# Performance work log

Hardware: AMD Instinct MI355X
Metric: run time of the kernel (lower is better)

## Reference

```python
import jax, jax.numpy as jnp
import numpy as np

H, KD, VD, KNN = 8, 64, 64, 128
D, FC, N, S = 512, 2048, 4, 1024
GW_DEC, GW_ENC = 0.5, 0.5
EPS = 1e-5
SCALE = float(np.sqrt(KD))


def _layer_norm(x):
    # nn.LayerNorm(out_dim, eps=1e-5, elementwise_affine=False)
    m = jnp.mean(x, -1, keepdims=True)
    v = jnp.var(x, -1, keepdims=True)
    return (x - m) * jax.lax.rsqrt(v + EPS)


def _mha(x, Wk, bk, Wv, bv, Wo, bo, att_graph, gw, mask, Wq=None, bq=None, q_in=None):
    # x: [N,S,D]; per-head projections stacked: Wk [H,D,Kd], Wv [H,D,Vd]
    key = jnp.einsum('nsd,hdk->hnsk', x, Wk) + bk[:, None, None, :]
    value = jnp.einsum('nsd,hdv->hnsv', x, Wv) + bv[:, None, None, :]
    if q_in is None:
        query = key  # self-attention: query = key (as in the torch code)
    else:
        query = jnp.einsum('nqd,hdk->hnqk', q_in, Wq) + bq[:, None, None, :]
    # broadcast-mul-sum in torch == batched matmul
    att = jnp.einsum('hnqk,hnsk->hnqs', query, key) / SCALE  # [H,N,Q,S]
    if mask:
        qlen, slen = att.shape[-2], att.shape[-1]
        causal = jnp.arange(slen)[None, :] <= jnp.arange(qlen)[:, None]
        att = jnp.where(causal, att, -jnp.inf)
    # knn sparsification: keep top-KNN per row, rest -> -inf (equiv to topk+scatter for distinct values)
    thresh = jax.lax.top_k(att, KNN)[0][..., -1:]
    att = jnp.where(att >= thresh, att, -jnp.inf)
    att = jax.nn.softmax(att, axis=-1)
    # blend with precomputed (softmaxed) graph attention
    att = gw * att_graph + (1.0 - gw) * att
    ctx = jnp.einsum('hnqs,hnsv->hnqv', att, value)  # [H,N,Q,Vd]
    ctx = jnp.transpose(ctx, (1, 2, 0, 3)).reshape(ctx.shape[1], ctx.shape[2], H * VD)
    return ctx @ Wo + bo


def setup_inputs() -> dict:
    key = jax.random.key(0)
    ks = jax.random.split(key, 22)
    p = lambda k, shp: (0.02 * jax.random.normal(k, shp)).astype(jnp.float32)
    return {
        'z': jax.random.normal(ks[0], (N, S, D), jnp.float32),
        'y': jax.random.normal(ks[1], (N, S, D), jnp.float32),
        'graph_dec': jax.random.normal(ks[2], (S, S), jnp.float32),
        'graph_enc': jax.random.normal(ks[3], (S, S), jnp.float32),
        'dec_Wk': p(ks[4], (H, D, KD)), 'dec_bk': p(ks[5], (H, KD)),
        'dec_Wv': p(ks[6], (H, D, VD)), 'dec_bv': p(ks[7], (H, VD)),
        'dec_Wo': p(ks[8], (H * VD, D)), 'dec_bo': p(ks[9], (D,)),
        'enc_Wk': p(ks[10], (H, D, KD)), 'enc_bk': p(ks[11], (H, KD)),
        'enc_Wq': p(ks[12], (H, D, KD)), 'enc_bq': p(ks[13], (H, KD)),
        'enc_Wv': p(ks[14], (H, D, VD)), 'enc_bv': p(ks[15], (H, VD)),
        'enc_Wo': p(ks[16], (H * VD, D)), 'enc_bo': p(ks[17], (D,)),
        'fc_W1': p(ks[18], (D, FC)), 'fc_b1': p(ks[19], (FC,)),
        'fc_W2': p(ks[20], (FC, D)), 'fc_b2': p(ks[21], (D,)),
    }


def reference(z, y, graph_dec, graph_enc, dec_Wk, dec_bk, dec_Wv, dec_bv, dec_Wo, dec_bo, enc_Wk, enc_bk, enc_Wq, enc_bq, enc_Wv, enc_bv, enc_Wo, enc_bo, fc_W1, fc_b1, fc_W2, fc_b2):
    # graphs are row-softmaxed at construction time in the torch module
    gdec = jax.nn.softmax(graph_dec, axis=-1)
    genc = jax.nn.softmax(graph_enc, axis=-1)
    # 1) masked decoder self-attention on y
    h = _mha(y, dec_Wk, dec_bk, dec_Wv, dec_bv, dec_Wo, dec_bo, gdec, GW_DEC, True)
    h = _layer_norm(h + y)
    # 2) encoder-decoder attention: keys/values from z, query from h via query_keys (query_key=True)
    h2 = _mha(z, enc_Wk, enc_bk, enc_Wv, enc_bv, enc_Wo, enc_bo, genc, GW_ENC, False, enc_Wq, enc_bq, h)
    h2 = _layer_norm(h2 + h)
    # 3) two-layer MLP
    h3 = jax.nn.relu(h2 @ fc_W1 + fc_b1) @ fc_W2 + fc_b2
    return _layer_norm(h3 + h2)
```

## Files before the change

### kernel.cpp

```cpp
#include <hip/hip_runtime.h>
#include <stdint.h>

typedef short short8 __attribute__((ext_vector_type(8)));
typedef short short4v __attribute__((ext_vector_type(4)));
typedef float floatx4 __attribute__((ext_vector_type(4)));
typedef unsigned uint4v __attribute__((ext_vector_type(4)));

#define H_  8
#define NB_ 4
#define S_  1024
#define D_  512
#define KD_ 64

__device__ __forceinline__ short f2bf(float f){
    unsigned u = __builtin_bit_cast(unsigned, f);
    u += 0x7fffu + ((u>>16)&1u);
    return (short)(u>>16);
}
__device__ __forceinline__ float wred_addf(float x){
    #pragma unroll
    for(int o=32;o>0;o>>=1) x += __shfl_xor(x,o,64);
    return x;
}
__device__ __forceinline__ float wred_maxf(float x){
    #pragma unroll
    for(int o=32;o>0;o>>=1) x = fmaxf(x,__shfl_xor(x,o,64));
    return x;
}
__device__ __forceinline__ unsigned umaxu(unsigned a, unsigned b){ return a>b?a:b; }
__device__ __forceinline__ unsigned uminu(unsigned a, unsigned b){ return a<b?a:b; }

template<int CTRL, int RMASK, int BC>
__device__ __forceinline__ unsigned dppu(unsigned x){
    return (unsigned)__builtin_amdgcn_update_dpp(0, (int)x, CTRL, RMASK, 0xf, BC);
}
template<int CTRL, int RMASK>
__device__ __forceinline__ unsigned dppu_m1(unsigned x){
    return (unsigned)__builtin_amdgcn_update_dpp((int)0xFFFFFFFF, (int)x, CTRL, RMASK, 0xf, 0);
}
__device__ __forceinline__ unsigned wsum_dpp_u(unsigned x){
    x += dppu<0x111,0xf,1>(x);
    x += dppu<0x112,0xf,1>(x);
    x += dppu<0x114,0xf,1>(x);
    x += dppu<0x118,0xf,1>(x);
    x += dppu<0x142,0xa,0>(x);
    x += dppu<0x143,0xc,0>(x);
    return (unsigned)__builtin_amdgcn_readlane((int)x, 63);
}
__device__ __forceinline__ unsigned wmax_dpp_u(unsigned x){
    x = umaxu(x, dppu<0x111,0xf,1>(x));
    x = umaxu(x, dppu<0x112,0xf,1>(x));
    x = umaxu(x, dppu<0x114,0xf,1>(x));
    x = umaxu(x, dppu<0x118,0xf,1>(x));
    x = umaxu(x, dppu<0x142,0xa,0>(x));
    x = umaxu(x, dppu<0x143,0xc,0>(x));
    return (unsigned)__builtin_amdgcn_readlane((int)x, 63);
}
__device__ __forceinline__ unsigned wmin_dpp_u(unsigned x){
    x = uminu(x, dppu_m1<0x111,0xf>(x));
    x = uminu(x, dppu_m1<0x112,0xf>(x));
    x = uminu(x, dppu_m1<0x114,0xf>(x));
    x = uminu(x, dppu_m1<0x118,0xf>(x));
    x = uminu(x, dppu_m1<0x142,0xa>(x));
    x = uminu(x, dppu_m1<0x143,0xc>(x));
    return (unsigned)__builtin_amdgcn_readlane((int)x, 63);
}
__device__ __forceinline__ float addu_f(float a, unsigned b){
    return a + __builtin_bit_cast(float, b);
}
__device__ __forceinline__ float wsum_dpp_f(float x){
    x = addu_f(x, dppu<0x111,0xf,1>(__builtin_bit_cast(unsigned,x)));
    x = addu_f(x, dppu<0x112,0xf,1>(__builtin_bit_cast(unsigned,x)));
    x = addu_f(x, dppu<0x114,0xf,1>(__builtin_bit_cast(unsigned,x)));
    x = addu_f(x, dppu<0x118,0xf,1>(__builtin_bit_cast(unsigned,x)));
    x = addu_f(x, dppu<0x142,0xa,0>(__builtin_bit_cast(unsigned,x)));
    x = addu_f(x, dppu<0x143,0xc,0>(__builtin_bit_cast(unsigned,x)));
    return __builtin_bit_cast(float, (unsigned)__builtin_amdgcn_readlane((int)__builtin_bit_cast(unsigned, x), 63));
}
__device__ __forceinline__ unsigned cvt_pk_bf16(float a, float b){
    unsigned r;
    asm("v_cvt_pk_bf16_f32 %0, %1, %2" : "=v"(r) : "v"(a), "v"(b));
    return r;
}
__device__ __forceinline__ unsigned count128(const unsigned (&kv)[16], unsigned mid){
    unsigned cv = 0u;
    #pragma unroll
    for(int j=0;j<8;j++) cv += (unsigned)(kv[j] >= mid);
    unsigned cs = 0u;
    #pragma unroll
    for(int j=8;j<16;j++) cs += (unsigned)__popcll(__ballot(kv[j] >= mid));
    return wsum_dpp_u(cv) + cs;
}

__global__ __launch_bounds__(256) void prep_kernel(
    const float* __restrict__ dWk, const float* __restrict__ dWv,
    const float* __restrict__ eWk, const float* __restrict__ eWv, const float* __restrict__ eWq,
    const float* __restrict__ dWo, const float* __restrict__ eWo,
    const float* __restrict__ W1, const float* __restrict__ W2,
    const float* __restrict__ y, const float* __restrict__ z,
    const float* __restrict__ g0, const float* __restrict__ g1,
    short* __restrict__ wKVd, short* __restrict__ wKVe, short* __restrict__ wQet,
    short* __restrict__ oWod, short* __restrict__ oWoe,
    short* __restrict__ oW1, short* __restrict__ oW2,
    short* __restrict__ y_bf, short* __restrict__ z_bf,
    short* __restrict__ og0, short* __restrict__ og1)
{
    __shared__ float t[32][33];
    int id = blockIdx.x;
    int tid = threadIdx.x;
    if(id < 1280){
        int zz = id >> 5; int rem = id & 31; int by = rem >> 1, bx = rem & 1;
        int w = zz>>3, h = zz&7;
        const float* src; short* dst;
        if(w==0){ src = dWk + h*32768; dst = wKVd + h*65536; }
        else if(w==1){ src = dWv + h*32768; dst = wKVd + h*65536 + 32768; }
        else if(w==2){ src = eWk + h*32768; dst = wKVe + h*65536; }
        else if(w==3){ src = eWv + h*32768; dst = wKVe + h*65536 + 32768; }
        else { src = eWq + h*32768; dst = wQet + h*32768; }
        int c0 = bx*32, r0 = by*32;
        int r = tid>>3, cq = (tid&7)*4;
        #pragma unroll
        for(int i=0;i<4;i++) t[r][cq+i] = src[(r0+r)*64 + c0+cq+i];
        __syncthreads();
        int c = tid>>3, rq = (tid&7)*4;
        #pragma unroll
        for(int i=0;i<4;i++) dst[(c0+c)*512 + r0+rq+i] = f2bf(t[rq+i][c]);
    } else if(id < 3840){
        int id2 = id - 1280;
        const float* src; short* dst; int R, C, c0, r0;
        if(id2 < 512){
            src = (id2<256)? dWo : eWo; dst = (id2<256)? oWod : oWoe;
            int tt = id2 & 255; R = 512; C = 512;
            c0 = (tt&15)*32; r0 = (tt>>4)*32;
        } else if(id2 < 1536){
            src = W1; dst = oW1; int tt = id2 - 512; R = 512; C = 2048;
            c0 = (tt&63)*32; r0 = (tt>>6)*32;
        } else {
            src = W2; dst = oW2; int tt = id2 - 1536; R = 2048; C = 512;
            c0 = (tt&15)*32; r0 = (tt>>4)*32;
        }
        int r = tid>>3, cq = (tid&7)*4;
        #pragma unroll
        for(int i=0;i<4;i++) t[r][cq+i] = src[(long)(r0+r)*C + c0+cq+i];
        __syncthreads();
        int c = tid>>3, rq = (tid&7)*4;
        #pragma unroll
        for(int i=0;i<4;i++) dst[(long)(c0+c)*R + r0+rq+i] = f2bf(t[rq+i][c]);
    } else if(id < 7936){
        int tt = id - 3840;
        int bx = tt & 2047, by = tt >> 11;
        const float* in = by ? z : y;
        short* out = by ? z_bf : y_bf;
        int i = (bx*256 + tid)*4;
        floatx4 v = *(const floatx4*)(in + i);
        short4v r;
        #pragma unroll
        for(int j=0;j<4;j++) r[j] = f2bf(v[j]);
        *(short4v*)(out + i) = r;
    } else {
        int tt = id - 7936;
        int row = tt & 1023, by = tt >> 10;
        const float* g = by ? g1 : g0;
        short* o = by ? og1 : og0;
        const float* gr = g + (long)row*S_;
        short* orow = o + (long)row*S_;
        int wave = tid>>6, lane = tid&63;
        float* red = &t[0][0];
        float v[4]; float mx = -3.0e38f;
        #pragma unroll
        for(int i=0;i<4;i++){ v[i] = gr[tid + 256*i]; mx = fmaxf(mx, v[i]); }
        mx = wred_maxf(mx);
        if(lane==0) red[wave] = mx;
        __syncthreads();
        mx = fmaxf(fmaxf(red[0],red[1]), fmaxf(red[2],red[3]));
        float s = 0.f;
        #pragma unroll
        for(int i=0;i<4;i++){ v[i] = __expf(v[i]-mx); s += v[i]; }
        s = wred_addf(s);
        if(lane==0) red[4+wave] = s;
        __syncthreads();
        s = red[4]+red[5]+red[6]+red[7];
        float inv = 0.5f/s;
        #pragma unroll
        for(int i=0;i<4;i++) orow[tid + 256*i] = f2bf(v[i]*inv);
    }
}

__global__ __launch_bounds__(256) void gemm_projkv_kernel(
    const short* __restrict__ Ay, const short* __restrict__ Az,
    const short* __restrict__ Bd, const short* __restrict__ Be,
    const float* __restrict__ dbk, const float* __restrict__ dbv,
    const float* __restrict__ ebk, const float* __restrict__ ebv,
    short* __restrict__ Kd, short* __restrict__ Vd,
    short* __restrict__ Ke, short* __restrict__ Ve)
{
    __shared__ short As[64*32];
    __shared__ short Bs[128*32];
    int z = blockIdx.z; int enc = z>>3; int zl = z&7;
    const short* A  = enc ? Az : Ay;
    const short* Bb = (enc ? Be : Bd) + zl*65536;
    const float* b1 = enc ? ebk : dbk;
    const float* b2 = enc ? ebv : dbv;
    short* o1 = enc ? Ke : Kd;
    short* o2 = enc ? Ve : Vd;
    int m0 = blockIdx.x*64;
    int tid = threadIdx.x, wave = tid>>6, lane = tid&63, quad = lane>>4, nl = lane&15;
    int wm = (wave&1)*32, wn = (wave>>1)*64;
    floatx4 acc[2][4];
    #pragma unroll
    for(int i=0;i<2;i++)
        #pragma unroll
        for(int j=0;j<4;j++) acc[i][j] = (floatx4){0.f,0.f,0.f,0.f};
    int r = tid>>2, c = (tid&3)*8;
    for(int k0=0;k0<512;k0+=32){
        __syncthreads();
        __builtin_amdgcn_global_load_lds(
            (const __attribute__((address_space(1))) unsigned*)(A + (long)(m0 + r)*512 + k0 + c),
            (__attribute__((address_space(3))) unsigned*)((char*)As + wave*1024), 16, 0, 0);
        #pragma unroll
        for(int i=0;i<2;i++)
            __builtin_amdgcn_global_load_lds(
                (const __attribute__((address_space(1))) unsigned*)(Bb + (long)(r + i*64)*512 + k0 + c),
                (__attribute__((address_space(3))) unsigned*)((char*)Bs + i*4096 + wave*1024), 16, 0, 0);
        __syncthreads();
        short8 af[2], bfr[4];
        #pragma unroll
        for(int i=0;i<2;i++) af[i] = *(const short8*)(As + (wm + i*16 + nl)*32 + quad*8);
        #pragma unroll
        for(int j=0;j<4;j++) bfr[j] = *(const short8*)(Bs + (wn + j*16 + nl)*32 + quad*8);
        #pragma unroll
        for(int i=0;i<2;i++)
            #pragma unroll
            for(int j=0;j<4;j++)
                acc[i][j] = __builtin_amdgcn_mfma_f32_16x16x32_bf16(af[i],bfr[j],acc[i][j],0,0,0);
    }
    #pragma unroll
    for(int j=0;j<4;j++){
        int n = wn + j*16 + nl;
        float bv = (n >= 64) ? b2[zl*64 + n - 64] : b1[zl*64 + n];
        #pragma unroll
        for(int i=0;i<2;i++){
            #pragma unroll
            for(int rr=0;rr<4;rr++){
                int m = m0 + wm + i*16 + quad*4 + rr;
                float v = acc[i][j][rr] + bv;
                long zb = (long)(zl*NB_ + (m>>10));
                if(n >= 64) o2[ (zb*KD_ + (n-64))*S_ + (m&1023) ] = f2bf(v);
                else        o1[ (zb*S_ + (m&1023))*KD_ + n ] = f2bf(v);
            }
        }
    }
}

__global__ __launch_bounds__(256) void gemm_projq_kernel(
    const short* __restrict__ A, const short* __restrict__ Bt,
    const float* __restrict__ b1, short* __restrict__ o1)
{
    __shared__ short As[64*32];
    __shared__ short Bs[64*32];
    int z = blockIdx.z;
    int m0 = blockIdx.x*64;
    const short* Bb = Bt + (long)z*(64*512);
    int tid = threadIdx.x, wave = tid>>6, lane = tid&63, quad = lane>>4, nl = lane&15;
    int wm = (wave&1)*32, wn = (wave>>1)*32;
    floatx4 acc[2][2];
    #pragma unroll
    for(int i=0;i<2;i++)
        #pragma unroll
        for(int j=0;j<2;j++) acc[i][j] = (floatx4){0.f,0.f,0.f,0.f};
    int r = tid>>2, c = (tid&3)*8;
    for(int k0=0;k0<512;k0+=32){
        __syncthreads();
        __builtin_amdgcn_global_load_lds(
            (const __attribute__((address_space(1))) unsigned*)(A + (long)(m0 + r)*512 + k0 + c),
            (__attribute__((address_space(3))) unsigned*)((char*)As + wave*1024), 16, 0, 0);
        __builtin_amdgcn_global_load_lds(
            (const __attribute__((address_space(1))) unsigned*)(Bb + (long)r*512 + k0 + c),
            (__attribute__((address_space(3))) unsigned*)((char*)Bs + wave*1024), 16, 0, 0);
        __syncthreads();
        short8 af[2], bfr[2];
        #pragma unroll
        for(int i=0;i<2;i++) af[i] = *(const short8*)(As + (wm + i*16 + nl)*32 + quad*8);
        #pragma unroll
        for(int j=0;j<2;j++) bfr[j] = *(const short8*)(Bs + (wn + j*16 + nl)*32 + quad*8);
        #pragma unroll
        for(int i=0;i<2;i++)
            #pragma unroll
            for(int j=0;j<2;j++)
                acc[i][j] = __builtin_amdgcn_mfma_f32_16x16x32_bf16(af[i],bfr[j],acc[i][j],0,0,0);
    }
    #pragma unroll
    for(int j=0;j<2;j++){
        int n = wn + j*16 + nl;
        float bv = b1[z*64 + n];
        #pragma unroll
        for(int i=0;i<2;i++){
            #pragma unroll
            for(int rr=0;rr<4;rr++){
                int m = m0 + wm + i*16 + quad*4 + rr;
                float v = acc[i][j][rr] + bv;
                long zb = (long)(z*NB_ + (m>>10));
                o1[ (zb*S_ + (m&1023))*KD_ + n ] = f2bf(v);
            }
        }
    }
}

template<int TM, int TN, int OUTBF, int RELU>
__global__ __launch_bounds__(256) void gemm_big_kernel(
    const short* __restrict__ A, const short* __restrict__ Bt, const float* __restrict__ bias,
    void* __restrict__ out, int M, int N, int K)
{
    __shared__ short As[TM*32];
    __shared__ short Bs[TN*32];
    int m0 = blockIdx.x*TM, n0 = blockIdx.y*TN;
    int tid = threadIdx.x, wave = tid>>6, lane = tid&63, quad = lane>>4, nl = lane&15;
    constexpr int MI = TM/32, NI = TN/32;
    int wm = (wave&1)*(TM/2), wn = (wave>>1)*(TN/2);
    floatx4 acc[MI][NI];
    #pragma unroll
    for(int i=0;i<MI;i++)
        #pragma unroll
        for(int j=0;j<NI;j++) acc[i][j] = (floatx4){0.f,0.f,0.f,0.f};

    int r = tid>>2, c = (tid&3)*8;
    for(int k0=0;k0<K;k0+=32){
        __syncthreads();
        #pragma unroll
        for(int i=0;i<TM/64;i++)
            __builtin_amdgcn_global_load_lds(
                (const __attribute__((address_space(1))) unsigned*)(A + (long)(m0 + r + i*64)*K + k0 + c),
                (__attribute__((address_space(3))) unsigned*)((char*)As + i*4096 + wave*1024),
                16, 0, 0);
        #pragma unroll
        for(int i=0;i<TN/64;i++)
            __builtin_amdgcn_global_load_lds(
                (const __attribute__((address_space(1))) unsigned*)(Bt + (long)(n0 + r + i*64)*K + k0 + c),
                (__attribute__((address_space(3))) unsigned*)((char*)Bs + i*4096 + wave*1024),
                16, 0, 0);
        __syncthreads();
        short8 af[MI], bfr[NI];
        #pragma unroll
        for(int i=0;i<MI;i++) af[i] = *(const short8*)(As + (wm + i*16 + nl)*32 + quad*8);
        #pragma unroll
        for(int j=0;j<NI;j++) bfr[j] = *(const short8*)(Bs + (wn + j*16 + nl)*32 + quad*8);
        #pragma unroll
        for(int i=0;i<MI;i++)
            #pragma unroll
            for(int j=0;j<NI;j++)
                acc[i][j] = __builtin_amdgcn_mfma_f32_16x16x32_bf16(af[i],bfr[j],acc[i][j],0,0,0);
    }
    #pragma unroll
    for(int j=0;j<NI;j++){
        int n = n0 + wn + j*16 + nl;
        float bv = bias[n];
        #pragma unroll
        for(int i=0;i<MI;i++){
            #pragma unroll
            for(int rr=0;rr<4;rr++){
                int m = m0 + wm + i*16 + quad*4 + rr;
                float v = acc[i][j][rr] + bv;
                if(RELU) v = fmaxf(v, 0.f);
                if(OUTBF) ((short*)out)[(long)m*N + n] = f2bf(v);
                else      ((float*)out)[(long)m*N + n] = v;
            }
        }
    }
}

template<int OUTB>
__global__ __launch_bounds__(1024) void gemm_ln_kernel(
    const short* __restrict__ A, const short* __restrict__ Bt,
    const float* __restrict__ bias, const float* __restrict__ res,
    float* __restrict__ outf, short* __restrict__ outb, int K)
{
    __shared__ short As[16*32];
    __shared__ short Bs[512*32];
    __shared__ float redn[2][16][16];
    int m0 = blockIdx.x*16;
    int tid = threadIdx.x, wave = tid>>6, lane = tid&63, quad = lane>>4, nl = lane&15;
    int wn = wave*32;
    floatx4 acc[2];
    acc[0] = (floatx4){0.f,0.f,0.f,0.f};
    acc[1] = (floatx4){0.f,0.f,0.f,0.f};
    int r = tid>>2, c = (tid&3)*8;
    for(int k0=0;k0<K;k0+=32){
        __syncthreads();
        if(wave==0)
            __builtin_amdgcn_global_load_lds(
                (const __attribute__((address_space(1))) unsigned*)(A + (long)(m0 + (lane>>2))*K + k0 + (lane&3)*8),
                (__attribute__((address_space(3))) unsigned*)((char*)As), 16, 0, 0);
        #pragma unroll
        for(int i=0;i<2;i++)
            __builtin_amdgcn_global_load_lds(
                (const __attribute__((address_space(1))) unsigned*)(Bt + (long)(r + i*256)*K + k0 + c),
                (__attribute__((address_space(3))) unsigned*)((char*)Bs + i*16384 + wave*1024), 16, 0, 0);
        __syncthreads();
        short8 af = *(const short8*)(As + nl*32 + quad*8);
        short8 b0 = *(const short8*)(Bs + (wn + nl)*32 + quad*8);
        short8 b1 = *(const short8*)(Bs + (wn + 16 + nl)*32 + quad*8);
        acc[0] = __builtin_amdgcn_mfma_f32_16x16x32_bf16(af,b0,acc[0],0,0,0);
        acc[1] = __builtin_amdgcn_mfma_f32_16x16x32_bf16(af,b1,acc[1],0,0,0);
    }
    float t[2][4];
    #pragma unroll
    for(int j=0;j<2;j++){
        int n = wn + j*16 + nl;
        float bv = bias[n];
        #pragma unroll
        for(int rr=0;rr<4;rr++){
            int m = quad*4 + rr;
            t[j][rr] = acc[j][rr] + bv + res[(long)(m0+m)*512 + n];
        }
    }
    #pragma unroll
    for(int rr=0;rr<4;rr++){
        float s  = t[0][rr] + t[1][rr];
        float s2 = t[0][rr]*t[0][rr] + t[1][rr]*t[1][rr];
        #pragma unroll
        for(int o=1;o<16;o<<=1){ s += __shfl_xor(s,o,16); s2 += __shfl_xor(s2,o,16); }
        if(nl==0){
            redn[0][quad*4+rr][wave] = s;
            redn[1][quad*4+rr][wave] = s2;
        }
    }
    __syncthreads();
    #pragma unroll
    for(int rr=0;rr<4;rr++){
        int row = quad*4 + rr;
        float s = 0.f, s2 = 0.f;
        #pragma unroll
        for(int b=0;b<4;b++){
            floatx4 p  = *(const floatx4*)&redn[0][row][b*4];
            floatx4 p2 = *(const floatx4*)&redn[1][row][b*4];
            s  += p[0]+p[1]+p[2]+p[3];
            s2 += p2[0]+p2[1]+p2[2]+p2[3];
        }
        float mean = s*(1.f/512.f);
        float var = s2*(1.f/512.f) - mean*mean;
        float rs = rsqrtf(var + 1e-5f);
        #pragma unroll
        for(int j=0;j<2;j++){
            int n = wn + j*16 + nl;
            float o = (t[j][rr] - mean)*rs;
            outf[(long)(m0+row)*512 + n] = o;
            if(OUTB) outb[(long)(m0+row)*512 + n] = f2bf(o);
        }
    }
}

__global__ __launch_bounds__(512,6) void attn_kernel(
    const short* __restrict__ Qb, const short* __restrict__ Kb, const short* __restrict__ Vt,
    const short* __restrict__ graph, short* __restrict__ ctx, int causal)
{
    __shared__ short attb[16*1024];
    __shared__ float pbuf[16*68];
    int hn = blockIdx.x, qt = blockIdx.y;
    int h = hn>>2, n = hn&3;
    int q0 = qt*16;
    int tid=threadIdx.x, wave=tid>>6, lane=tid&63, quad=lane>>4, nl=lane&15;

    if(causal){
        uint4v fv = (uint4v){0xff80ff80u,0xff80ff80u,0xff80ff80u,0xff80ff80u};
        #pragma unroll
        for(int i=0;i<4;i++) *(uint4v*)((char*)attb + tid*16 + i*8192) = fv;
        __syncthreads();
    }

    const short* Qp = Qb + ((long)hn*S_ + q0 + nl)*KD_ + quad*8;
    short8 aq0 = *(const short8*)(Qp);
    short8 aq1 = *(const short8*)(Qp + 32);
    const short* Kp = Kb + (long)hn*S_*KD_;
    int stmax = causal ? qt : 63;
    for(int st=wave; st<=stmax; st+=8){
        const short* kp = Kp + (st*16 + nl)*KD_ + quad*8;
        short8 b0 = *(const short8*)(kp);
        short8 b1 = *(const short8*)(kp + 32);
        floatx4 cc = (floatx4){0.f,0.f,0.f,0.f};
        cc = __builtin_amdgcn_mfma_f32_16x16x32_bf16(aq0,b0,cc,0,0,0);
        cc = __builtin_amdgcn_mfma_f32_16x16x32_bf16(aq1,b1,cc,0,0,0);
        int s = st*16 + nl;
        #pragma unroll
        for(int rr=0;rr<4;rr++){
            int q = quad*4 + rr;
            short val = f2bf(cc[rr]*0.125f);
            if(causal && s > q0 + q) val = (short)0xff80;
            attb[q*1024 + ((s + 8*q)&1023)] = val;
        }
    }
    __syncthreads();

    #pragma unroll 1
    for(int rp=0; rp<2; ++rp){
        int q = wave*2 + rp;
        int qg = q0 + q;
        short* rowp = attb + q*1024;
        int sb = lane*16;
        int p0 = (sb + 8*q) & 1023;
        const short* grow = graph + (long)qg*1024 + sb;
        uint4v g0 = *(const uint4v*)(grow);
        uint4v g1 = *(const uint4v*)(grow + 8);
        uint4v u0 = *(const uint4v*)(rowp + p0);
        uint4v u1 = *(const uint4v*)(rowp + ((p0+8)&1023));
        unsigned pr[8];
        #pragma unroll
        for(int i=0;i<4;i++){ pr[i] = u0[i]; pr[4+i] = u1[i]; }
        unsigned kv[16];
        #pragma unroll
        for(int i=0;i<8;i++){
            unsigned u = pr[i];
            unsigned kp = u ^ (0x80008000u + ((u>>15)&0x00010001u)*0x7fffu);
            kv[2*i]   = kp & 0xffffu;
            kv[2*i+1] = kp >> 16;
        }
        unsigned a0 = umaxu(kv[0],kv[1]),  a1 = umaxu(kv[2],kv[3]);
        unsigned a2 = umaxu(kv[4],kv[5]),  a3 = umaxu(kv[6],kv[7]);
        unsigned a4 = umaxu(kv[8],kv[9]),  a5 = umaxu(kv[10],kv[11]);
        unsigned a6 = umaxu(kv[12],kv[13]),a7 = umaxu(kv[14],kv[15]);
        unsigned mk = umaxu(umaxu(umaxu(a0,a1),umaxu(a2,a3)), umaxu(umaxu(a4,a5),umaxu(a6,a7)));
        unsigned mks = wmax_dpp_u(mk);
        unsigned lmin = wmin_dpp_u(mk);
        unsigned lo, hi, clo, chi;
        {
            unsigned cnt = count128(kv, lmin);
            if(cnt >= 128u){
                lo = lmin; clo = cnt;
                hi = (cnt == 128u) ? (lmin + 1u) : (mks + 1u); chi = 0u;
            } else {
                lo = 0u; clo = 1024u; hi = lmin; chi = cnt;
            }
        }
        int it = 0;
        while(hi - lo > 1u){
            unsigned span = hi - lo;
            unsigned mid;
            if((it++ & 1) == 0){
                float fr = (float)(clo - 128u) / (float)(clo - chi);
                unsigned off = (unsigned)(fr * (float)span);
                off = off < 1u ? 1u : off;
                off = off > span - 1u ? span - 1u : off;
                mid = lo + off;
            } else {
                mid = lo + (span >> 1);
            }
            unsigned cnt = count128(kv, mid);
            if(cnt >= 128u){ lo = mid; clo = cnt; if(cnt == 128u) break; }
            else { hi = mid; chi = cnt; }
        }
        unsigned uo = (mks & 0x8000u) ? ((mks & 0x7fffu)<<16) : ((~mks)<<16);
        float mxf = __builtin_bit_cast(float, uo);
        float ev[16]; float sm = 0.f;
        #pragma unroll
        for(int i=0;i<8;i++){
            float f0 = __builtin_bit_cast(float, pr[i] << 16);
            float f1 = __builtin_bit_cast(float, pr[i] & 0xffff0000u);
            float e0 = __expf(f0 - mxf);
            float e1 = __expf(f1 - mxf);
            e0 = (kv[2*i]   >= lo) ? e0 : 0.f;
            e1 = (kv[2*i+1] >= lo) ? e1 : 0.f;
            ev[2*i] = e0; ev[2*i+1] = e1;
            sm += e0 + e1;
        }
        sm = wsum_dpp_f(sm);
        float inv = 0.5f / sm;
        uint4v w0, w1;
        #pragma unroll
        for(int i=0;i<4;i++){
            float gl0 = __builtin_bit_cast(float, g0[i] << 16);
            float gh0 = __builtin_bit_cast(float, g0[i] & 0xffff0000u);
            w0[i] = cvt_pk_bf16(fmaf(ev[2*i], inv, gl0), fmaf(ev[2*i+1], inv, gh0));
            float gl1 = __builtin_bit_cast(float, g1[i] << 16);
            float gh1 = __builtin_bit_cast(float, g1[i] & 0xffff0000u);
            w1[i] = cvt_pk_bf16(fmaf(ev[8+2*i], inv, gl1), fmaf(ev[8+2*i+1], inv, gh1));
        }
        *(uint4v*)(rowp + p0) = w0;
        *(uint4v*)(rowp + ((p0+8)&1023)) = w1;
    }
    __syncthreads();

    int vh = wave & 3, sh = wave >> 2;
    int v0 = vh*16;
    const short* Vp = Vt + ((long)hn*KD_ + v0 + nl)*S_;
    floatx4 o4 = (floatx4){0.f,0.f,0.f,0.f};
    int arow = nl;
    int sbase = sh*512;
    for(int s0=sbase; s0<sbase+512; s0+=32){
        int cs = (s0 + quad*8 + 8*arow) & 1023;
        short8 ap = *(const short8*)(attb + arow*1024 + cs);
        short8 bv = *(const short8*)(Vp + s0 + quad*8);
        o4 = __builtin_amdgcn_mfma_f32_16x16x32_bf16(ap,bv,o4,0,0,0);
    }
    if(sh==1){
        #pragma unroll
        for(int rr=0;rr<4;rr++) pbuf[(quad*4+rr)*68 + v0 + nl] = o4[rr];
    }
    __syncthreads();
    if(sh==0){
        #pragma unroll
        for(int rr=0;rr<4;rr++){
            int q = quad*4 + rr;
            float v = o4[rr] + pbuf[q*68 + v0 + nl];
            ctx[ ((long)(n*S_ + q0 + q))*512 + h*KD_ + v0 + nl ] = f2bf(v);
        }
    }
}

extern "C" void kernel_launch(void* const* d_in, const int* in_sizes, int n_in,
                              void* d_out, int out_size, void* d_ws, size_t ws_size,
                              hipStream_t stream)
{
    const float* z         = (const float*)d_in[0];
    const float* y         = (const float*)d_in[1];
    const float* graph_dec = (const float*)d_in[2];
    const float* graph_enc = (const float*)d_in[3];
    const float* dec_Wk = (const float*)d_in[4];  const float* dec_bk = (const float*)d_in[5];
    const float* dec_Wv = (const float*)d_in[6];  const float* dec_bv = (const float*)d_in[7];
    const float* dec_Wo = (const float*)d_in[8];  const float* dec_bo = (const float*)d_in[9];
    const float* enc_Wk = (const float*)d_in[10]; const float* enc_bk = (const float*)d_in[11];
    const float* enc_Wq = (const float*)d_in[12]; const float* enc_bq = (const float*)d_in[13];
    const float* enc_Wv = (const float*)d_in[14]; const float* enc_bv = (const float*)d_in[15];
    const float* enc_Wo = (const float*)d_in[16]; const float* enc_bo = (const float*)d_in[17];
    const float* fc_W1  = (const float*)d_in[18]; const float* fc_b1  = (const float*)d_in[19];
    const float* fc_W2  = (const float*)d_in[20]; const float* fc_b2  = (const float*)d_in[21];

    char* ws = (char*)d_ws;
    short* gdec  = (short*)(ws + 0x0000000);
    short* genc  = (short*)(ws + 0x0400000);
    short* y_bf  = (short*)(ws + 0x0800000);
    short* z_bf  = (short*)(ws + 0x0C00000);
    short* Kdec  = (short*)(ws + 0x1000000);
    short* Vtdec = (short*)(ws + 0x1400000);
    short* Kenc  = (short*)(ws + 0x1800000);
    short* Vtenc = (short*)(ws + 0x1C00000);
    short* Qenc  = (short*)(ws + 0x2000000);
    short* ctx   = (short*)(ws + 0x2400000);
    float* hbuf  = (float*)(ws + 0x3000000);
    short* h_bf  = (short*)(ws + 0x3800000);
    float* h2    = (float*)(ws + 0x3C00000);
    short* h2_bf = (short*)(ws + 0x4400000);
    short* fc1   = (short*)(ws + 0x4800000);
    short* wKVd  = (short*)(ws + 0x5800000);
    short* wKVe  = (short*)(ws + 0x5900000);
    short* wQet  = (short*)(ws + 0x5A00000);
    short* wOdt  = (short*)(ws + 0x5A80000);
    short* wOet  = (short*)(ws + 0x5B00000);
    short* wF1t  = (short*)(ws + 0x5B80000);
    short* wF2t  = (short*)(ws + 0x5D80000);
    float* outp  = (float*)d_out;

    prep_kernel<<<dim3(9984),dim3(256),0,stream>>>(
        dec_Wk, dec_Wv, enc_Wk, enc_Wv, enc_Wq, dec_Wo, enc_Wo, fc_W1, fc_W2,
        y, z, graph_dec, graph_enc,
        wKVd, wKVe, wQet, wOdt, wOet, wF1t, wF2t, y_bf, z_bf, gdec, genc);
    gemm_projkv_kernel<<<dim3(64,1,16),dim3(256),0,stream>>>(
        y_bf, z_bf, wKVd, wKVe, dec_bk, dec_bv, enc_bk, enc_bv,
        Kdec, Vtdec, Kenc, Vtenc);
    attn_kernel<<<dim3(32,64),dim3(512),0,stream>>>(Kdec, Kdec, Vtdec, gdec, ctx, 1);
    gemm_ln_kernel<1><<<dim3(256),dim3(1024),0,stream>>>(ctx, wOdt, dec_bo, y, hbuf, h_bf, 512);
    gemm_projq_kernel<<<dim3(64,1,8),dim3(256),0,stream>>>(h_bf, wQet, enc_bq, Qenc);
    attn_kernel<<<dim3(32,64),dim3(512),0,stream>>>(Qenc, Kenc, Vtenc, genc, ctx, 0);
    gemm_ln_kernel<1><<<dim3(256),dim3(1024),0,stream>>>(ctx, wOet, enc_bo, hbuf, h2, h2_bf, 512);
    gemm_big_kernel<128,128,1,1><<<dim3(32,16),dim3(256),0,stream>>>(h2_bf, wF1t, fc_b1, fc1, 4096, 2048, 512);
    gemm_ln_kernel<0><<<dim3(256),dim3(1024),0,stream>>>(fc1, wF2t, fc_b2, h2, outp, (short*)0, 2048);
}
```

Measured before the change: 417.6 us.

## Split fused GEMM+LayerNorm into tiled GEMM plus separate LN kernel; simplify top-k bisection

Replaces the 16-row GEMM+LayerNorm kernel, which reloads the full 512-wide weight panel for every 16 rows, with the general tiled gemm_big_kernel writing fp32 to a temporary buffer, followed by a standalone row LayerNorm kernel. This raises weight reuse and gives a better-shaped grid for the output projections and the FC2 GEMM. The cost is an extra fp32 round trip through global memory and three more kernel launches. The top-k threshold search in attention also drops the alternating interpolation step and uses plain bisection.

```diff
diff --git a/kernel.cpp b/kernel.cpp
--- a/kernel.cpp
+++ b/kernel.cpp
@@ -368,87 +368,6 @@
     }
 }
 
-template<int OUTB>
-__global__ __launch_bounds__(1024) void gemm_ln_kernel(
-    const short* __restrict__ A, const short* __restrict__ Bt,
-    const float* __restrict__ bias, const float* __restrict__ res,
-    float* __restrict__ outf, short* __restrict__ outb, int K)
-{
-    __shared__ short As[16*32];
-    __shared__ short Bs[512*32];
-    __shared__ float redn[2][16][16];
-    int m0 = blockIdx.x*16;
-    int tid = threadIdx.x, wave = tid>>6, lane = tid&63, quad = lane>>4, nl = lane&15;
-    int wn = wave*32;
-    floatx4 acc[2];
-    acc[0] = (floatx4){0.f,0.f,0.f,0.f};
-    acc[1] = (floatx4){0.f,0.f,0.f,0.f};
-    int r = tid>>2, c = (tid&3)*8;
-    for(int k0=0;k0<K;k0+=32){
-        __syncthreads();
-        if(wave==0)
-            __builtin_amdgcn_global_load_lds(
-                (const __attribute__((address_space(1))) unsigned*)(A + (long)(m0 + (lane>>2))*K + k0 + (lane&3)*8),
-                (__attribute__((address_space(3))) unsigned*)((char*)As), 16, 0, 0);
-        #pragma unroll
-        for(int i=0;i<2;i++)
-            __builtin_amdgcn_global_load_lds(
-                (const __attribute__((address_space(1))) unsigned*)(Bt + (long)(r + i*256)*K + k0 + c),
-                (__attribute__((address_space(3))) unsigned*)((char*)Bs + i*16384 + wave*1024), 16, 0, 0);
-        __syncthreads();
-        short8 af = *(const short8*)(As + nl*32 + quad*8);
-        short8 b0 = *(const short8*)(Bs + (wn + nl)*32 + quad*8);
-        short8 b1 = *(const short8*)(Bs + (wn + 16 + nl)*32 + quad*8);
-        acc[0] = __builtin_amdgcn_mfma_f32_16x16x32_bf16(af,b0,acc[0],0,0,0);
-        acc[1] = __builtin_amdgcn_mfma_f32_16x16x32_bf16(af,b1,acc[1],0,0,0);
-    }
-    float t[2][4];
-    #pragma unroll
-    for(int j=0;j<2;j++){
-        int n = wn + j*16 + nl;
-        float bv = bias[n];
-        #pragma unroll
-        for(int rr=0;rr<4;rr++){
-            int m = quad*4 + rr;
-            t[j][rr] = acc[j][rr] + bv + res[(long)(m0+m)*512 + n];
-        }
-    }
-    #pragma unroll
-    for(int rr=0;rr<4;rr++){
-        float s  = t[0][rr] + t[1][rr];
-        float s2 = t[0][rr]*t[0][rr] + t[1][rr]*t[1][rr];
-        #pragma unroll
-        for(int o=1;o<16;o<<=1){ s += __shfl_xor(s,o,16); s2 += __shfl_xor(s2,o,16); }
-        if(nl==0){
-            redn[0][quad*4+rr][wave] = s;
-            redn[1][quad*4+rr][wave] = s2;
-        }
-    }
-    __syncthreads();
-    #pragma unroll
-    for(int rr=0;rr<4;rr++){
-        int row = quad*4 + rr;
-        float s = 0.f, s2 = 0.f;
-        #pragma unroll
-        for(int b=0;b<4;b++){
-            floatx4 p  = *(const floatx4*)&redn[0][row][b*4];
-            floatx4 p2 = *(const floatx4*)&redn[1][row][b*4];
-            s  += p[0]+p[1]+p[2]+p[3];
-            s2 += p2[0]+p2[1]+p2[2]+p2[3];
-        }
-        float mean = s*(1.f/512.f);
-        float var = s2*(1.f/512.f) - mean*mean;
-        float rs = rsqrtf(var + 1e-5f);
-        #pragma unroll
-        for(int j=0;j<2;j++){
-            int n = wn + j*16 + nl;
-            float o = (t[j][rr] - mean)*rs;
-            outf[(long)(m0+row)*512 + n] = o;
-            if(OUTB) outb[(long)(m0+row)*512 + n] = f2bf(o);
-        }
-    }
-}
-
 __global__ __launch_bounds__(512,6) void attn_kernel(
     const short* __restrict__ Qb, const short* __restrict__ Kb, const short* __restrict__ Vt,
     const short* __restrict__ graph, short* __restrict__ ctx, int causal)
@@ -520,32 +439,17 @@
         unsigned mk = umaxu(umaxu(umaxu(a0,a1),umaxu(a2,a3)), umaxu(umaxu(a4,a5),umaxu(a6,a7)));
         unsigned mks = wmax_dpp_u(mk);
         unsigned lmin = wmin_dpp_u(mk);
-        unsigned lo, hi, clo, chi;
+        unsigned lo, hi;
         {
             unsigned cnt = count128(kv, lmin);
-            if(cnt >= 128u){
-                lo = lmin; clo = cnt;
-                hi = (cnt == 128u) ? (lmin + 1u) : (mks + 1u); chi = 0u;
-            } else {
-                lo = 0u; clo = 1024u; hi = lmin; chi = cnt;
-            }
-        }
-        int it = 0;
+            if(cnt >= 128u){ lo = lmin; hi = (cnt == 128u) ? (lmin + 1u) : (mks + 1u); }
+            else           { lo = 0u;   hi = lmin; }
+        }
         while(hi - lo > 1u){
-            unsigned span = hi - lo;
-            unsigned mid;
-            if((it++ & 1) == 0){
-                float fr = (float)(clo - 128u) / (float)(clo - chi);
-                unsigned off = (unsigned)(fr * (float)span);
-                off = off < 1u ? 1u : off;
-                off = off > span - 1u ? span - 1u : off;
-                mid = lo + off;
-            } else {
-                mid = lo + (span >> 1);
-            }
+            unsigned mid = (lo + hi) >> 1;
             unsigned cnt = count128(kv, mid);
-            if(cnt >= 128u){ lo = mid; clo = cnt; if(cnt == 128u) break; }
-            else { hi = mid; chi = cnt; }
+            if(cnt >= 128u){ lo = mid; if(cnt == 128u) break; }
+            else hi = mid;
         }
         unsigned uo = (mks & 0x8000u) ? ((mks & 0x7fffu)<<16) : ((~mks)<<16);
         float mxf = __builtin_bit_cast(float, uo);
@@ -603,6 +507,29 @@
             ctx[ ((long)(n*S_ + q0 + q))*512 + h*KD_ + v0 + nl ] = f2bf(v);
         }
     }
+}
+
+__global__ __launch_bounds__(256) void ln_kernel(const float* __restrict__ x, const float* __restrict__ res,
+                                                 float* __restrict__ outf, short* __restrict__ outb){
+    long row = blockIdx.x;
+    const float* xr = x + row*D_;
+    const float* rr = res + row*D_;
+    int tid = threadIdx.x, wave = tid>>6, lane = tid&63;
+    float t0 = xr[tid] + rr[tid];
+    float t1 = xr[tid+256] + rr[tid+256];
+    float s = t0 + t1, s2 = t0*t0 + t1*t1;
+    __shared__ float red[8];
+    s = wred_addf(s); s2 = wred_addf(s2);
+    if(lane==0){ red[wave] = s; red[4+wave] = s2; }
+    __syncthreads();
+    s  = red[0]+red[1]+red[2]+red[3];
+    s2 = red[4]+red[5]+red[6]+red[7];
+    float mean = s*(1.f/512.f);
+    float var = s2*(1.f/512.f) - mean*mean;
+    float rs = rsqrtf(var + 1e-5f);
+    float o0 = (t0-mean)*rs, o1 = (t1-mean)*rs;
+    if(outf){ outf[row*D_+tid] = o0; outf[row*D_+tid+256] = o1; }
+    if(outb){ outb[row*D_+tid] = f2bf(o0); outb[row*D_+tid+256] = f2bf(o1); }
 }
 
 extern "C" void kernel_launch(void* const* d_in, const int* in_sizes, int n_in,
@@ -634,6 +561,7 @@
     short* Vtenc = (short*)(ws + 0x1C00000);
     short* Qenc  = (short*)(ws + 0x2000000);
     short* ctx   = (short*)(ws + 0x2400000);
+    float* tmp   = (float*)(ws + 0x2800000);
     float* hbuf  = (float*)(ws + 0x3000000);
     short* h_bf  = (short*)(ws + 0x3800000);
     float* h2    = (float*)(ws + 0x3C00000);
@@ -648,18 +576,22 @@
     short* wF2t  = (short*)(ws + 0x5D80000);
     float* outp  = (float*)d_out;
 
-    prep_kernel<<<dim3(9984),dim3(256),0,stream>>>(
+    dim3 B(256);
+    prep_kernel<<<dim3(9984),B,0,stream>>>(
         dec_Wk, dec_Wv, enc_Wk, enc_Wv, enc_Wq, dec_Wo, enc_Wo, fc_W1, fc_W2,
         y, z, graph_dec, graph_enc,
         wKVd, wKVe, wQet, wOdt, wOet, wF1t, wF2t, y_bf, z_bf, gdec, genc);
-    gemm_projkv_kernel<<<dim3(64,1,16),dim3(256),0,stream>>>(
+    gemm_projkv_kernel<<<dim3(64,1,16),B,0,stream>>>(
         y_bf, z_bf, wKVd, wKVe, dec_bk, dec_bv, enc_bk, enc_bv,
         Kdec, Vtdec, Kenc, Vtenc);
     attn_kernel<<<dim3(32,64),dim3(512),0,stream>>>(Kdec, Kdec, Vtdec, gdec, ctx, 1);
-    gemm_ln_kernel<1><<<dim3(256),dim3(1024),0,stream>>>(ctx, wOdt, dec_bo, y, hbuf, h_bf, 512);
-    gemm_projq_kernel<<<dim3(64,1,8),dim3(256),0,stream>>>(h_bf, wQet, enc_bq, Qenc);
+    gemm_big_kernel<64,128,0,0><<<dim3(64,4),B,0,stream>>>(ctx, wOdt, dec_bo, tmp, 4096, 512, 512);
+    ln_kernel<<<dim3(4096),B,0,stream>>>(tmp, y, hbuf, h_bf);
+    gemm_projq_kernel<<<dim3(64,1,8),B,0,stream>>>(h_bf, wQet, enc_bq, Qenc);
     attn_kernel<<<dim3(32,64),dim3(512),0,stream>>>(Qenc, Kenc, Vtenc, genc, ctx, 0);
-    gemm_ln_kernel<1><<<dim3(256),dim3(1024),0,stream>>>(ctx, wOet, enc_bo, hbuf, h2, h2_bf, 512);
-    gemm_big_kernel<128,128,1,1><<<dim3(32,16),dim3(256),0,stream>>>(h2_bf, wF1t, fc_b1, fc1, 4096, 2048, 512);
-    gemm_ln_kernel<0><<<dim3(256),dim3(1024),0,stream>>>(fc1, wF2t, fc_b2, h2, outp, (short*)0, 2048);
-}
+    gemm_big_kernel<64,128,0,0><<<dim3(64,4),B,0,stream>>>(ctx, wOet, enc_bo, tmp, 4096, 512, 512);
+    ln_kernel<<<dim3(4096),B,0,stream>>>(tmp, hbuf, h2, h2_bf);
+    gemm_big_kernel<128,128,1,1><<<dim3(32,16),B,0,stream>>>(h2_bf, wF1t, fc_b1, fc1, 4096, 2048, 512);
+    gemm_big_kernel<64,128,0,0><<<dim3(64,4),B,0,stream>>>(fc1, wF2t, fc_b2, tmp, 4096, 512, 2048);
+    ln_kernel<<<dim3(4096),B,0,stream>>>(tmp, h2, outp, (short*)0);
+}
```

Result: faster. 376.3 us (-9.9%).
